# Kernel optimization log

Hardware: AMD Instinct MI355X
Metric: run time of the kernel (lower is better)

## Reference

```python
import jax, jax.numpy as jnp
import numpy as np

DIM = 2048   # token width; == heads*head_dim
H, DH = 16, 128
B, S = 1, 2048
E, K = 4, 2          # routed experts, top-k
HID = 5632           # per-expert SwiGLU hidden: round256(int(2*(4*DIM)/3))
HS = 2816            # shared expert hidden: round256(int(2*(2*DIM)/3))


def setup_inputs() -> dict:
    key = jax.random.key(0)
    ks = jax.random.split(key, 24)
    def g(i, shape, s=0.02):
        return jax.random.normal(ks[i], shape, dtype=jnp.float32) * s
    return {
        "image_tokens": jax.random.normal(ks[0], (B, S, DIM), dtype=jnp.float32),
        "adaln_input": jax.random.normal(ks[1], (B, DIM), dtype=jnp.float32),
        "W_ada": g(2, (DIM, 6 * DIM)), "b_ada": g(3, (6 * DIM,)),
        "Wq": g(4, (DIM, DIM)), "bq": g(5, (DIM,)),
        "Wk": g(6, (DIM, DIM)), "bk": g(7, (DIM,)),
        "Wv": g(8, (DIM, DIM)), "bv": g(9, (DIM,)),
        "q_rms_w": jnp.ones((DIM,), jnp.float32) + g(10, (DIM,)),
        "k_rms_w": jnp.ones((DIM,), jnp.float32) + g(11, (DIM,)),
        "Wo": g(12, (DIM, DIM)), "bo": g(13, (DIM,)),
        "gate_w": g(14, (E, DIM)),
        "We1": g(15, (E, DIM, HID)), "We3": g(16, (E, DIM, HID)), "We2": g(17, (E, HID, DIM)),
        "Ws1": g(18, (DIM, HS)), "Ws3": g(19, (DIM, HS)), "Ws2": g(20, (HS, DIM)),
    }


def _ln(x):  # LayerNorm, elementwise_affine=False, eps=1e-6
    m = jnp.mean(x, -1, keepdims=True)
    v = jnp.var(x, -1, keepdims=True)
    return (x - m) * jax.lax.rsqrt(v + 1e-6)


def _rms(x, w):  # RMSNorm with affine weight, eps=1e-5
    return x * jax.lax.rsqrt(jnp.mean(x * x, -1, keepdims=True) + 1e-5) * w


def reference(image_tokens, adaln_input, W_ada, b_ada, Wq, bq, Wk, bk, Wv, bv,
              q_rms_w, k_rms_w, Wo, bo, gate_w, We1, We3, We2, Ws1, Ws3, Ws2):
    # adaLN: SiLU -> Linear -> 6 chunks, each broadcast as [B,1,dim]
    mod = (jax.nn.silu(adaln_input) @ W_ada + b_ada)[:, None, :]
    sh_msa, sc_msa, g_msa, sh_mlp, sc_mlp, g_mlp = jnp.split(mod, 6, axis=-1)

    # attention branch
    x = _ln(image_tokens) * (1.0 + sc_msa) + sh_msa
    q = _rms(x @ Wq + bq, q_rms_w).reshape(B, S, H, DH)
    k = _rms(x @ Wk + bk, k_rms_w).reshape(B, S, H, DH)
    v = (x @ Wv + bv).reshape(B, S, H, DH)
    att = jax.nn.softmax(jnp.einsum('bihd,bjhd->bhij', q, k) / jnp.sqrt(jnp.float32(DH)), axis=-1)
    o = jnp.einsum('bhij,bjhd->bihd', att, v).reshape(B, S, DIM) @ Wo + bo
    img = g_msa * o + image_tokens

    # MoE SwiGLU FFN branch
    y = _ln(img) * (1.0 + sc_mlp) + sh_mlp
    xf = y.reshape(-1, DIM)                                   # [N, dim]
    scores = jax.nn.softmax(xf @ gate_w.T, axis=-1)           # [N, E]
    tw, ti = jax.lax.top_k(scores, K)                         # no top-k renorm (norm_topk_prob=False)
    comb = jnp.zeros((xf.shape[0], E), xf.dtype).at[jnp.arange(xf.shape[0])[:, None], ti].add(tw)
    h = jax.nn.silu(jnp.einsum('nd,edh->neh', xf, We1)) * jnp.einsum('nd,edh->neh', xf, We3)
    routed = jnp.einsum('neh,ehd,ne->nd', h, We2, comb)
    shared = (jax.nn.silu(xf @ Ws1) * (xf @ Ws3)) @ Ws2
    ff = (routed + shared).reshape(B, S, DIM)

    return g_mlp * ff + img
```

## Files before the change

### kernel.cpp

```cpp
#include <hip/hip_runtime.h>
#include <hip/hip_bf16.h>

typedef unsigned short u16;
typedef __bf16 bf16x8 __attribute__((ext_vector_type(8)));
typedef float f32x4 __attribute__((ext_vector_type(4)));
typedef unsigned short u16x8 __attribute__((ext_vector_type(8)));

constexpr int DIMC = 2048;
constexpr int SEQ = 2048;
constexpr int NHEAD = 16;
constexpr int HDIM = 128;
constexpr int NEXP = 4;
constexpr int HIDC = 5632;
constexpr int HSH = 2816;
constexpr int MOD6 = 6 * DIMC;
constexpr int RSTRIDE = 2304;

static __device__ __forceinline__ u16 f2bf(float f) {
  __hip_bfloat16 b = __float2bfloat16(f);
  return __builtin_bit_cast(u16, b);
}
static __device__ __forceinline__ float bf2f(u16 u) {
  unsigned int x = ((unsigned int)u) << 16;
  return __builtin_bit_cast(float, x);
}
static __device__ __forceinline__ float sigf(float x) { return 1.f / (1.f + __expf(-x)); }
static __device__ __forceinline__ void splitf(float f, u16& h, u16& l) {
  h = f2bf(f);
  l = f2bf(f - bf2f(h));
}

static __device__ __forceinline__ void gload16(const void* src, void* dst) {
  __builtin_amdgcn_global_load_lds((const __attribute__((address_space(1))) void*)src,
                                   (__attribute__((address_space(3))) void*)dst, 16, 0, 0);
}

static __device__ __forceinline__ void xcd_swz(int& bx, int& by, int& bz) {
  const int nx = gridDim.x, ny = gridDim.y;
  const int flat = blockIdx.x + nx * (blockIdx.y + ny * blockIdx.z);
  const int nwg = nx * ny * gridDim.z;
  const int swz = (flat & 7) * (nwg >> 3) + (flat >> 3);
  by = swz % ny;
  const int t = swz / ny;
  bx = t % nx;
  bz = t / nx;
}

static __device__ __forceinline__ float blockSum(float v) {
#pragma unroll
  for (int m = 1; m < 64; m <<= 1) v += __shfl_xor(v, m);
  __shared__ float s[4];
  int w = threadIdx.x >> 6;
  if ((threadIdx.x & 63) == 0) s[w] = v;
  __syncthreads();
  float r = s[0] + s[1] + s[2] + s[3];
  __syncthreads();
  return r;
}

__global__ __launch_bounds__(256) void k_transpose(const float* __restrict__ in, u16* __restrict__ out,
                                                   int R, int C, int ldin, size_t inz, size_t outz) {
  __shared__ __align__(16) float tile[32][33];
  const float* inp = in + (size_t)blockIdx.z * inz;
  u16* outp = out + (size_t)blockIdx.z * outz;
  int tx = threadIdx.x & 31, ty = threadIdx.x >> 5;
  int c0 = blockIdx.x * 32, r0 = blockIdx.y * 32;
#pragma unroll
  for (int i = 0; i < 32; i += 8)
    tile[ty + i][tx] = inp[(size_t)(r0 + ty + i) * ldin + c0 + tx];
  __syncthreads();
#pragma unroll
  for (int i = 0; i < 32; i += 8)
    outp[(size_t)(c0 + ty + i) * R + r0 + tx] = f2bf(tile[tx][ty + i]);
}

__global__ __launch_bounds__(256) void k_transpose_s(const float* __restrict__ in, u16* __restrict__ outh,
                                                     u16* __restrict__ outl, int R, int C, int ldin) {
  __shared__ __align__(16) float tile[32][33];
  int tx = threadIdx.x & 31, ty = threadIdx.x >> 5;
  int c0 = blockIdx.x * 32, r0 = blockIdx.y * 32;
#pragma unroll
  for (int i = 0; i < 32; i += 8)
    tile[ty + i][tx] = in[(size_t)(r0 + ty + i) * ldin + c0 + tx];
  __syncthreads();
#pragma unroll
  for (int i = 0; i < 32; i += 8) {
    float v = tile[tx][ty + i];
    u16 h, l;
    splitf(v, h, l);
    size_t idx = (size_t)(c0 + ty + i) * R + r0 + tx;
    outh[idx] = h;
    outl[idx] = l;
  }
}

__global__ __launch_bounds__(256) void k_adaln_p(const float* __restrict__ a, const float* __restrict__ W,
                                                 float* __restrict__ partial) {
  __shared__ float sa[128];
  int tid = threadIdx.x, slice = blockIdx.y;
  if (tid < 128) { float v = a[slice * 128 + tid]; sa[tid] = v * sigf(v); }
  __syncthreads();
  int j = blockIdx.x * 256 + tid;
  float acc = 0.f;
#pragma unroll 4
  for (int d = 0; d < 128; ++d) acc += sa[d] * W[(size_t)(slice * 128 + d) * MOD6 + j];
  partial[(size_t)slice * MOD6 + j] = acc;
}
__global__ __launch_bounds__(256) void k_adaln_r(const float* __restrict__ partial, const float* __restrict__ b,
                                                 float* __restrict__ mod) {
  int j = blockIdx.x * 256 + threadIdx.x;
  float acc = b[j];
#pragma unroll
  for (int s = 0; s < 16; ++s) acc += partial[(size_t)s * MOD6 + j];
  mod[j] = acc;
}

__global__ __launch_bounds__(256) void k_ln_mod_split(const float* __restrict__ X, const float* __restrict__ mod,
                                                      int shOff, int scOff, u16* __restrict__ outh,
                                                      u16* __restrict__ outl) {
  int row = blockIdx.x, tid = threadIdx.x;
  const float4* x4 = (const float4*)(X + (size_t)row * DIMC);
  float4 v0 = x4[tid * 2], v1 = x4[tid * 2 + 1];
  float s = v0.x + v0.y + v0.z + v0.w + v1.x + v1.y + v1.z + v1.w;
  float ss = v0.x * v0.x + v0.y * v0.y + v0.z * v0.z + v0.w * v0.w +
             v1.x * v1.x + v1.y * v1.y + v1.z * v1.z + v1.w * v1.w;
  s = blockSum(s);
  ss = blockSum(ss);
  float mean = s * (1.f / DIMC);
  float var = ss * (1.f / DIMC) - mean * mean;
  float rstd = rsqrtf(var + 1e-6f);
  const float* sh = mod + shOff;
  const float* sc = mod + scOff;
  int c = tid * 8;
  float xv[8] = {v0.x, v0.y, v0.z, v0.w, v1.x, v1.y, v1.z, v1.w};
  u16x8 oh, ol;
#pragma unroll
  for (int e = 0; e < 8; ++e) {
    float v = (xv[e] - mean) * rstd * (1.f + sc[c + e]) + sh[c + e];
    u16 h, l;
    splitf(v, h, l);
    oh[e] = h;
    ol[e] = l;
  }
  *(u16x8*)(outh + (size_t)row * DIMC + c) = oh;
  *(u16x8*)(outl + (size_t)row * DIMC + c) = ol;
}

__global__ __launch_bounds__(256) void k_ln_mod(const float* __restrict__ X, const float* __restrict__ mod,
                                                int shOff, int scOff, u16* __restrict__ out) {
  int row = blockIdx.x, tid = threadIdx.x;
  const float4* x4 = (const float4*)(X + (size_t)row * DIMC);
  float4 v0 = x4[tid * 2], v1 = x4[tid * 2 + 1];
  float s = v0.x + v0.y + v0.z + v0.w + v1.x + v1.y + v1.z + v1.w;
  float ss = v0.x * v0.x + v0.y * v0.y + v0.z * v0.z + v0.w * v0.w +
             v1.x * v1.x + v1.y * v1.y + v1.z * v1.z + v1.w * v1.w;
  s = blockSum(s);
  ss = blockSum(ss);
  float mean = s * (1.f / DIMC);
  float var = ss * (1.f / DIMC) - mean * mean;
  float rstd = rsqrtf(var + 1e-6f);
  const float* sh = mod + shOff;
  const float* sc = mod + scOff;
  int c = tid * 8;
  float xv[8] = {v0.x, v0.y, v0.z, v0.w, v1.x, v1.y, v1.z, v1.w};
  u16x8 o;
#pragma unroll
  for (int e = 0; e < 8; ++e) o[e] = f2bf((xv[e] - mean) * rstd * (1.f + sc[c + e]) + sh[c + e]);
  *(u16x8*)(out + (size_t)row * DIMC + c) = o;
}

__global__ __launch_bounds__(256) void k_rms_split(const float* __restrict__ X, int ldin,
                                                   const float* __restrict__ w, float scale,
                                                   u16* __restrict__ outh, u16* __restrict__ outl) {
  int row = blockIdx.x, tid = threadIdx.x;
  const float4* x4 = (const float4*)(X + (size_t)row * ldin);
  float4 v0 = x4[tid * 2], v1 = x4[tid * 2 + 1];
  float ss = v0.x * v0.x + v0.y * v0.y + v0.z * v0.z + v0.w * v0.w +
             v1.x * v1.x + v1.y * v1.y + v1.z * v1.z + v1.w * v1.w;
  ss = blockSum(ss);
  float rstd = rsqrtf(ss * (1.f / DIMC) + 1e-5f) * scale;
  int c = tid * 8;
  float xv[8] = {v0.x, v0.y, v0.z, v0.w, v1.x, v1.y, v1.z, v1.w};
  u16x8 oh, ol;
#pragma unroll
  for (int e = 0; e < 8; ++e) {
    float v = xv[e] * rstd * w[c + e];
    u16 h, l;
    splitf(v, h, l);
    oh[e] = h;
    ol[e] = l;
  }
  *(u16x8*)(outh + (size_t)row * DIMC + c) = oh;
  *(u16x8*)(outl + (size_t)row * DIMC + c) = ol;
}

__global__ __launch_bounds__(256) void k_gate(const float* __restrict__ img, const float* __restrict__ mod,
                                              const float* __restrict__ gw, float* __restrict__ comb) {
  int n = blockIdx.x, tid = threadIdx.x;
  const float4* x4 = (const float4*)(img + (size_t)n * DIMC);
  float4 v0 = x4[tid * 2], v1 = x4[tid * 2 + 1];
  float s = v0.x + v0.y + v0.z + v0.w + v1.x + v1.y + v1.z + v1.w;
  float ss = v0.x * v0.x + v0.y * v0.y + v0.z * v0.z + v0.w * v0.w +
             v1.x * v1.x + v1.y * v1.y + v1.z * v1.z + v1.w * v1.w;
  s = blockSum(s);
  ss = blockSum(ss);
  float mean = s * (1.f / DIMC);
  float var = ss * (1.f / DIMC) - mean * mean;
  float rstd = rsqrtf(var + 1e-6f);
  const float* sh = mod + 3 * DIMC;
  const float* sc = mod + 4 * DIMC;
  int c = tid * 8;
  float xv[8] = {v0.x, v0.y, v0.z, v0.w, v1.x, v1.y, v1.z, v1.w};
  float y[8];
#pragma unroll
  for (int e = 0; e < 8; ++e) y[e] = (xv[e] - mean) * rstd * (1.f + sc[c + e]) + sh[c + e];
  float accs[NEXP];
#pragma unroll
  for (int ex = 0; ex < NEXP; ++ex) {
    float a = 0.f;
#pragma unroll
    for (int e = 0; e < 8; ++e) a += y[e] * gw[(size_t)ex * DIMC + c + e];
    accs[ex] = blockSum(a);
  }
  if (tid == 0) {
    float mx = fmaxf(fmaxf(accs[0], accs[1]), fmaxf(accs[2], accs[3]));
    float ex0 = __expf(accs[0] - mx), ex1 = __expf(accs[1] - mx);
    float ex2 = __expf(accs[2] - mx), ex3 = __expf(accs[3] - mx);
    float inv = 1.f / (ex0 + ex1 + ex2 + ex3);
    float v[4] = {ex0 * inv, ex1 * inv, ex2 * inv, ex3 * inv};
    int i1 = 0;
    for (int e = 1; e < 4; ++e)
      if (v[e] > v[i1]) i1 = e;
    int i2 = -1;
    for (int e = 0; e < 4; ++e) {
      if (e == i1) continue;
      if (i2 < 0 || v[e] > v[i2]) i2 = e;
    }
    for (int e = 0; e < 4; ++e) comb[(size_t)n * 4 + e] = (e == i1 || e == i2) ? v[e] : 0.f;
  }
}

__global__ __launch_bounds__(256) void k_route(const float* __restrict__ comb, int* __restrict__ gidx,
                                               float* __restrict__ cw, int* __restrict__ Mpad) {
  int wid = threadIdx.x >> 6, lane = threadIdx.x & 63;
  int base = 0;
  for (int c = 0; c < SEQ; c += 64) {
    int n = c + lane;
    float w = comb[(size_t)n * NEXP + wid];
    bool sel = w > 0.f;
    unsigned long long mask = __ballot(sel);
    int pos = __popcll(mask & ((1ull << lane) - 1ull));
    if (sel) {
      gidx[wid * RSTRIDE + base + pos] = n;
      cw[wid * RSTRIDE + base + pos] = w;
    }
    base += __popcll(mask);
  }
  int padded = (base + 127) & ~127;
  for (int i = base + lane; i < padded; i += 64) {
    gidx[wid * RSTRIDE + i] = -1;
    cw[wid * RSTRIDE + i] = 0.f;
  }
  if (lane == 0) Mpad[wid] = padded;
}

__global__ __launch_bounds__(256, 2) void k_gemmD(const u16* __restrict__ A, const u16* __restrict__ BT,
                                                  int M, int N, int K, float* __restrict__ Cf) {
  int bx, by, bzz;
  xcd_swz(bx, by, bzz);
  __shared__ __align__(16) u16 As[2][8192], Bs[2][8192];
  const int tid = threadIdx.x, wid = tid >> 6, lane = tid & 63;
  const int l16 = lane & 15, g = lane >> 4;
  const int wr = wid >> 1, wc = wid & 1;
  const int m0 = by * 128, n0 = bx * 128;
  const int srow = lane >> 2, scol = (lane & 3) * 8;
  const u16* aS0 = A + (size_t)(m0 + wid * 32 + srow) * K + scol;
  const u16* aS1 = aS0 + (size_t)16 * K;
  const u16* bS0 = BT + (size_t)(n0 + wid * 32 + srow) * K + scol;
  const u16* bS1 = bS0 + (size_t)16 * K;

  const f32x4 zero4 = {0.f, 0.f, 0.f, 0.f};
  f32x4 acc[4][4];
#pragma unroll
  for (int mi = 0; mi < 4; ++mi)
#pragma unroll
    for (int ni = 0; ni < 4; ++ni) acc[mi][ni] = zero4;

  auto stage = [&](int b, int k0) {
    gload16(aS0 + k0, &As[b][wid * 1024]);
    gload16(aS1 + k0, &As[b][wid * 1024 + 512]);
    gload16(aS0 + k0 + 32, &As[b][4096 + wid * 1024]);
    gload16(aS1 + k0 + 32, &As[b][4096 + wid * 1024 + 512]);
    gload16(bS0 + k0, &Bs[b][wid * 1024]);
    gload16(bS1 + k0, &Bs[b][wid * 1024 + 512]);
    gload16(bS0 + k0 + 32, &Bs[b][4096 + wid * 1024]);
    gload16(bS1 + k0 + 32, &Bs[b][4096 + wid * 1024 + 512]);
  };
  auto compute = [&](int b) {
#pragma unroll
    for (int hh = 0; hh < 2; ++hh) {
      const u16* Asrc = &As[b][hh * 4096];
      const u16* Bsrc = &Bs[b][hh * 4096];
      bf16x8 af[4], bfr[4];
#pragma unroll
      for (int mi = 0; mi < 4; ++mi)
        af[mi] = *(const bf16x8*)(&Asrc[(wr * 64 + mi * 16 + l16) * 32 + g * 8]);
#pragma unroll
      for (int ni = 0; ni < 4; ++ni)
        bfr[ni] = *(const bf16x8*)(&Bsrc[(wc * 64 + ni * 16 + l16) * 32 + g * 8]);
#pragma unroll
      for (int mi = 0; mi < 4; ++mi)
#pragma unroll
        for (int ni = 0; ni < 4; ++ni)
          acc[mi][ni] = __builtin_amdgcn_mfma_f32_16x16x32_bf16(af[mi], bfr[ni], acc[mi][ni], 0, 0, 0);
    }
  };

  stage(0, 0);
  __syncthreads();
  for (int k0 = 0; k0 < K; k0 += 128) {
    if (k0 + 64 < K) stage(1, k0 + 64);
    compute(0);
    __syncthreads();
    if (k0 + 128 < K) stage(0, k0 + 128);
    compute(1);
    __syncthreads();
  }

#pragma unroll
  for (int mi = 0; mi < 4; ++mi)
#pragma unroll
    for (int ni = 0; ni < 4; ++ni) {
      const int col = n0 + wc * 64 + ni * 16 + l16;
#pragma unroll
      for (int r = 0; r < 4; ++r) {
        const int row = m0 + wr * 64 + mi * 16 + g * 4 + r;
        Cf[(size_t)row * N + col] = acc[mi][ni][r];
      }
    }
}

template <int GATH>
__global__ __launch_bounds__(256, 2) void k_gemmUP(const u16* __restrict__ A, const u16* __restrict__ B1T0,
                                                   const u16* __restrict__ B3T0, size_t bzs, int N, int K,
                                                   const int* __restrict__ gidx0,
                                                   const float* __restrict__ cw0,
                                                   const int* __restrict__ Mp0, u16* __restrict__ G0,
                                                   size_t cz) {
  int bx, by, bz;
  xcd_swz(bx, by, bz);
  const int z = bz;
  const int m0 = by * 128;
  const int* gidxE = nullptr;
  const float* cwE = nullptr;
  if constexpr (GATH) {
    if (m0 >= Mp0[z]) return;
    gidxE = gidx0 + (size_t)z * RSTRIDE;
    cwE = cw0 + (size_t)z * RSTRIDE;
  }
  const u16* B1T = B1T0 + (size_t)z * bzs;
  const u16* B3T = B3T0 + (size_t)z * bzs;
  u16* G = G0 + (size_t)z * cz;

  __shared__ __align__(16) u16 As[8192], B1s[8192], B3s[8192];
  const int tid = threadIdx.x, wid = tid >> 6, lane = tid & 63;
  const int l16 = lane & 15, g = lane >> 4;
  const int wr = wid >> 1, wc = wid & 1;
  const int n0 = bx * 128;
  const int srow = lane >> 2, scol = (lane & 3) * 8;
  const int slot0 = m0 + wid * 32 + srow;
  int row0, row1;
  if constexpr (GATH) {
    int t0 = gidxE[slot0], t1 = gidxE[slot0 + 16];
    row0 = t0 < 0 ? 0 : t0;
    row1 = t1 < 0 ? 0 : t1;
  } else {
    row0 = slot0;
    row1 = slot0 + 16;
  }
  const u16* aS0 = A + (size_t)row0 * K + scol;
  const u16* aS1 = A + (size_t)row1 * K + scol;
  const u16* b1S0 = B1T + (size_t)(n0 + wid * 32 + srow) * K + scol;
  const u16* b1S1 = b1S0 + (size_t)16 * K;
  const u16* b3S0 = B3T + (size_t)(n0 + wid * 32 + srow) * K + scol;
  const u16* b3S1 = b3S0 + (size_t)16 * K;

  const f32x4 zero4 = {0.f, 0.f, 0.f, 0.f};
  f32x4 acc1[4][4], acc3[4][4];
#pragma unroll
  for (int mi = 0; mi < 4; ++mi)
#pragma unroll
    for (int ni = 0; ni < 4; ++ni) {
      acc1[mi][ni] = zero4;
      acc3[mi][ni] = zero4;
    }

  for (int k0 = 0; k0 < K; k0 += 64) {
    __syncthreads();
    gload16(aS0 + k0, &As[wid * 1024]);
    gload16(aS1 + k0, &As[wid * 1024 + 512]);
    gload16(aS0 + k0 + 32, &As[4096 + wid * 1024]);
    gload16(aS1 + k0 + 32, &As[4096 + wid * 1024 + 512]);
    gload16(b1S0 + k0, &B1s[wid * 1024]);
    gload16(b1S1 + k0, &B1s[wid * 1024 + 512]);
    gload16(b1S0 + k0 + 32, &B1s[4096 + wid * 1024]);
    gload16(b1S1 + k0 + 32, &B1s[4096 + wid * 1024 + 512]);
    gload16(b3S0 + k0, &B3s[wid * 1024]);
    gload16(b3S1 + k0, &B3s[wid * 1024 + 512]);
    gload16(b3S0 + k0 + 32, &B3s[4096 + wid * 1024]);
    gload16(b3S1 + k0 + 32, &B3s[4096 + wid * 1024 + 512]);
    __syncthreads();
#pragma unroll
    for (int hh = 0; hh < 2; ++hh) {
      const u16* Asrc = &As[hh * 4096];
      const u16* B1src = &B1s[hh * 4096];
      const u16* B3src = &B3s[hh * 4096];
      bf16x8 af[4], b1f[4], b3f[4];
#pragma unroll
      for (int mi = 0; mi < 4; ++mi)
        af[mi] = *(const bf16x8*)(&Asrc[(wr * 64 + mi * 16 + l16) * 32 + g * 8]);
#pragma unroll
      for (int ni = 0; ni < 4; ++ni) {
        b1f[ni] = *(const bf16x8*)(&B1src[(wc * 64 + ni * 16 + l16) * 32 + g * 8]);
        b3f[ni] = *(const bf16x8*)(&B3src[(wc * 64 + ni * 16 + l16) * 32 + g * 8]);
      }
#pragma unroll
      for (int mi = 0; mi < 4; ++mi)
#pragma unroll
        for (int ni = 0; ni < 4; ++ni) {
          acc1[mi][ni] = __builtin_amdgcn_mfma_f32_16x16x32_bf16(af[mi], b1f[ni], acc1[mi][ni], 0, 0, 0);
          acc3[mi][ni] = __builtin_amdgcn_mfma_f32_16x16x32_bf16(af[mi], b3f[ni], acc3[mi][ni], 0, 0, 0);
        }
    }
  }

#pragma unroll
  for (int mi = 0; mi < 4; ++mi)
#pragma unroll
    for (int ni = 0; ni < 4; ++ni) {
      const int col = n0 + wc * 64 + ni * 16 + l16;
#pragma unroll
      for (int r = 0; r < 4; ++r) {
        const int slot = m0 + wr * 64 + mi * 16 + g * 4 + r;
        float hv = bf2f(f2bf(acc1[mi][ni][r]));
        float sw = hv * sigf(hv);
        float val = sw * acc3[mi][ni][r];
        if constexpr (GATH) val = val * cwE[slot];
        G[(size_t)slot * N + col] = f2bf(val);
      }
    }
}

__global__ __launch_bounds__(256, 2) void k_gemmR2(const u16* __restrict__ A0, size_t az,
                                                   const u16* __restrict__ BT0, size_t bzs, int N, int K,
                                                   const int* __restrict__ gidx0,
                                                   const int* __restrict__ Mp0, float* __restrict__ ffA,
                                                   float* __restrict__ ffB) {
  int bx, by, bz;
  xcd_swz(bx, by, bz);
  const int z = bz;
  const int m0 = by * 128;
  if (m0 >= Mp0[z]) return;
  const int* gidxE = gidx0 + (size_t)z * RSTRIDE;
  const u16* A = A0 + (size_t)z * az;
  const u16* BT = BT0 + (size_t)z * bzs;
  float* ff = z ? ffB : ffA;

  __shared__ __align__(16) u16 As[2][8192], Bs[2][8192];
  const int tid = threadIdx.x, wid = tid >> 6, lane = tid & 63;
  const int l16 = lane & 15, g = lane >> 4;
  const int wr = wid >> 1, wc = wid & 1;
  const int n0 = bx * 128;
  const int srow = lane >> 2, scol = (lane & 3) * 8;
  const int slot0 = m0 + wid * 32 + srow;
  const u16* aS0 = A + (size_t)slot0 * K + scol;
  const u16* aS1 = A + (size_t)(slot0 + 16) * K + scol;
  const u16* bS0 = BT + (size_t)(n0 + wid * 32 + srow) * K + scol;
  const u16* bS1 = bS0 + (size_t)16 * K;

  const f32x4 zero4 = {0.f, 0.f, 0.f, 0.f};
  f32x4 acc[4][4];
#pragma unroll
  for (int mi = 0; mi < 4; ++mi)
#pragma unroll
    for (int ni = 0; ni < 4; ++ni) acc[mi][ni] = zero4;

  auto stage = [&](int b, int k0) {
    gload16(aS0 + k0, &As[b][wid * 1024]);
    gload16(aS1 + k0, &As[b][wid * 1024 + 512]);
    gload16(aS0 + k0 + 32, &As[b][4096 + wid * 1024]);
    gload16(aS1 + k0 + 32, &As[b][4096 + wid * 1024 + 512]);
    gload16(bS0 + k0, &Bs[b][wid * 1024]);
    gload16(bS1 + k0, &Bs[b][wid * 1024 + 512]);
    gload16(bS0 + k0 + 32, &Bs[b][4096 + wid * 1024]);
    gload16(bS1 + k0 + 32, &Bs[b][4096 + wid * 1024 + 512]);
  };
  auto compute = [&](int b) {
#pragma unroll
    for (int hh = 0; hh < 2; ++hh) {
      const u16* Asrc = &As[b][hh * 4096];
      const u16* Bsrc = &Bs[b][hh * 4096];
      bf16x8 af[4], bfr[4];
#pragma unroll
      for (int mi = 0; mi < 4; ++mi)
        af[mi] = *(const bf16x8*)(&Asrc[(wr * 64 + mi * 16 + l16) * 32 + g * 8]);
#pragma unroll
      for (int ni = 0; ni < 4; ++ni)
        bfr[ni] = *(const bf16x8*)(&Bsrc[(wc * 64 + ni * 16 + l16) * 32 + g * 8]);
#pragma unroll
      for (int mi = 0; mi < 4; ++mi)
#pragma unroll
        for (int ni = 0; ni < 4; ++ni)
          acc[mi][ni] = __builtin_amdgcn_mfma_f32_16x16x32_bf16(af[mi], bfr[ni], acc[mi][ni], 0, 0, 0);
    }
  };

  stage(0, 0);
  __syncthreads();
  for (int k0 = 0; k0 < K; k0 += 128) {
    if (k0 + 64 < K) stage(1, k0 + 64);
    compute(0);
    __syncthreads();
    if (k0 + 128 < K) stage(0, k0 + 128);
    compute(1);
    __syncthreads();
  }

#pragma unroll
  for (int mi = 0; mi < 4; ++mi)
#pragma unroll
    for (int ni = 0; ni < 4; ++ni) {
      const int col = n0 + wc * 64 + ni * 16 + l16;
#pragma unroll
      for (int r = 0; r < 4; ++r) {
        const int slot = m0 + wr * 64 + mi * 16 + g * 4 + r;
        int t = gidxE[slot];
        if (t >= 0) ff[(size_t)t * N + col] += acc[mi][ni][r];
      }
    }
}

template <int MODE>
__global__ __launch_bounds__(256, 2) void k_gemm3s(const u16* __restrict__ Ahg, const u16* __restrict__ Alg,
                                                   const u16* __restrict__ Bhg, const u16* __restrict__ Blg,
                                                   int M, int N, int K, float* __restrict__ Cf,
                                                   const float* __restrict__ bias0,
                                                   const float* __restrict__ bias1,
                                                   const float* __restrict__ bias2,
                                                   const float* __restrict__ gvec,
                                                   const float* __restrict__ resid) {
  int bxs, bys, bzs2;
  xcd_swz(bxs, bys, bzs2);
  __shared__ __align__(16) u16 Ahs[2][4096], Als[2][4096], Bhs[2][4096], Bls[2][4096];
  const int tid = threadIdx.x, wid = tid >> 6, lane = tid & 63;
  const int l16 = lane & 15, g = lane >> 4;
  const int wr = wid >> 1, wc = wid & 1;
  const int m0 = bys * 128, n0 = bxs * 128;
  const int srow = lane >> 2, scol = (lane & 3) * 8;
  const size_t aOff0 = (size_t)(m0 + wid * 32 + srow) * K + scol;
  const size_t aOff1 = aOff0 + (size_t)16 * K;
  const size_t bOff0 = (size_t)(n0 + wid * 32 + srow) * K + scol;
  const size_t bOff1 = bOff0 + (size_t)16 * K;

  const f32x4 zero4 = {0.f, 0.f, 0.f, 0.f};
  f32x4 acc[4][4];
#pragma unroll
  for (int mi = 0; mi < 4; ++mi)
#pragma unroll
    for (int ni = 0; ni < 4; ++ni) acc[mi][ni] = zero4;

  auto stage = [&](int b, int k0) {
    gload16(Ahg + aOff0 + k0, &Ahs[b][wid * 1024]);
    gload16(Ahg + aOff1 + k0, &Ahs[b][wid * 1024 + 512]);
    gload16(Alg + aOff0 + k0, &Als[b][wid * 1024]);
    gload16(Alg + aOff1 + k0, &Als[b][wid * 1024 + 512]);
    gload16(Bhg + bOff0 + k0, &Bhs[b][wid * 1024]);
    gload16(Bhg + bOff1 + k0, &Bhs[b][wid * 1024 + 512]);
    gload16(Blg + bOff0 + k0, &Bls[b][wid * 1024]);
    gload16(Blg + bOff1 + k0, &Bls[b][wid * 1024 + 512]);
  };
  auto compute = [&](int b) {
    bf16x8 bhf[4], blf[4];
#pragma unroll
    for (int ni = 0; ni < 4; ++ni) {
      bhf[ni] = *(const bf16x8*)(&Bhs[b][(wc * 64 + ni * 16 + l16) * 32 + g * 8]);
      blf[ni] = *(const bf16x8*)(&Bls[b][(wc * 64 + ni * 16 + l16) * 32 + g * 8]);
    }
#pragma unroll
    for (int mi = 0; mi < 4; ++mi) {
      bf16x8 ahf = *(const bf16x8*)(&Ahs[b][(wr * 64 + mi * 16 + l16) * 32 + g * 8]);
      bf16x8 alf = *(const bf16x8*)(&Als[b][(wr * 64 + mi * 16 + l16) * 32 + g * 8]);
#pragma unroll
      for (int ni = 0; ni < 4; ++ni) {
        acc[mi][ni] = __builtin_amdgcn_mfma_f32_16x16x32_bf16(alf, bhf[ni], acc[mi][ni], 0, 0, 0);
        acc[mi][ni] = __builtin_amdgcn_mfma_f32_16x16x32_bf16(ahf, blf[ni], acc[mi][ni], 0, 0, 0);
        acc[mi][ni] = __builtin_amdgcn_mfma_f32_16x16x32_bf16(ahf, bhf[ni], acc[mi][ni], 0, 0, 0);
      }
    }
  };

  stage(0, 0);
  __syncthreads();
  for (int k0 = 0; k0 < K; k0 += 64) {
    if (k0 + 32 < K) stage(1, k0 + 32);
    compute(0);
    __syncthreads();
    if (k0 + 64 < K) stage(0, k0 + 64);
    compute(1);
    __syncthreads();
  }

  const float* bp = bias0;
  if constexpr (MODE == 7) bp = (n0 < DIMC) ? bias0 : (n0 < 2 * DIMC ? bias1 : bias2);
#pragma unroll
  for (int mi = 0; mi < 4; ++mi)
#pragma unroll
    for (int ni = 0; ni < 4; ++ni) {
      const int col = n0 + wc * 64 + ni * 16 + l16;
      float bv = bp ? bp[col & (DIMC - 1)] : 0.f;
#pragma unroll
      for (int r = 0; r < 4; ++r) {
        const int row = m0 + wr * 64 + mi * 16 + g * 4 + r;
        float v = acc[mi][ni][r] + bv;
        if constexpr (MODE == 7) {
          Cf[(size_t)row * N + col] = v;
        } else {
          Cf[(size_t)row * N + col] = v * gvec[col] + resid[(size_t)row * N + col];
        }
      }
    }
}

__global__ __launch_bounds__(256, 3) void k_flash3(const u16* __restrict__ qh_g, const u16* __restrict__ ql_g,
                                                   const u16* __restrict__ kh_g, const u16* __restrict__ kl_g,
                                                   const u16* __restrict__ vth_g, const u16* __restrict__ vtl_g,
                                                   u16* __restrict__ oh_g, u16* __restrict__ ol_g) {
  __shared__ __align__(16) u16 Kh[4096], Kl[4096], Vh[128 * 40], Vl[128 * 40];
  __shared__ __align__(16) u16 Pah[4][16 * 40], Pal[4][16 * 40];
  const int tid = threadIdx.x, wid = tid >> 6, lane = tid & 63;
  const int l16 = lane & 15, g = lane >> 4;
  const int bid = blockIdx.x;
  const int h = (bid & 7) + ((bid >> 8) << 3);
  const int qb = (bid >> 3) & 31;
  const int r0 = qb * 64 + wid * 16;
  const size_t hOff = (size_t)h * HDIM;

  bf16x8 qfh[4], qfl[4];
#pragma unroll
  for (int kc = 0; kc < 4; ++kc) {
    const size_t qo = (size_t)(r0 + l16) * DIMC + hOff + kc * 32 + g * 8;
    qfh[kc] = *(const bf16x8*)(qh_g + qo);
    qfl[kc] = *(const bf16x8*)(ql_g + qo);
  }

  const int kr = tid >> 3, ke0 = (tid & 7) * 16;
  const int kswz = (kr & 7) << 4;
  const int kc0 = (ke0 * 2) ^ kswz, kc1 = (ke0 * 2 + 16) ^ kswz;
  char* khp = (char*)Kh + kr * 256;
  char* klp = (char*)Kl + kr * 256;
  const size_t kOff = (size_t)kr * DIMC + hOff + ke0;
  const int vr = tid >> 1, ve0 = (tid & 1) * 16;
  char* vhp = (char*)Vh + vr * 80 + ve0 * 2;
  char* vlp = (char*)Vl + vr * 80 + ve0 * 2;
  const size_t vOff = (size_t)(hOff + vr) * SEQ + ve0;

  u16x8 kH0, kH1, kL0, kL1, vH0, vH1, vL0, vL1;
  kH0 = *(const u16x8*)(kh_g + kOff);
  kH1 = *(const u16x8*)(kh_g + kOff + 8);
  kL0 = *(const u16x8*)(kl_g + kOff);
  kL1 = *(const u16x8*)(kl_g + kOff + 8);
  vH0 = *(const u16x8*)(vth_g + vOff);
  vH1 = *(const u16x8*)(vth_g + vOff + 8);
  vL0 = *(const u16x8*)(vtl_g + vOff);
  vL1 = *(const u16x8*)(vtl_g + vOff + 8);

  const f32x4 zero4 = {0.f, 0.f, 0.f, 0.f};
  f32x4 oacc[8];
#pragma unroll
  for (int db = 0; db < 8; ++db) oacc[db] = zero4;
  float mr[4], lr[4];
#pragma unroll
  for (int r = 0; r < 4; ++r) {
    mr[r] = -3.0e38f;
    lr[r] = 0.f;
  }

  for (int j0 = 0; j0 < SEQ; j0 += 32) {
    __syncthreads();
    *(u16x8*)(khp + kc0) = kH0;
    *(u16x8*)(khp + kc1) = kH1;
    *(u16x8*)(klp + kc0) = kL0;
    *(u16x8*)(klp + kc1) = kL1;
    *(u16x8*)(vhp) = vH0;
    *(u16x8*)(vhp + 16) = vH1;
    *(u16x8*)(vlp) = vL0;
    *(u16x8*)(vlp + 16) = vL1;
    __syncthreads();
    if (j0 + 32 < SEQ) {
      const size_t ko = kOff + (size_t)(j0 + 32) * DIMC;
      const size_t vo = vOff + j0 + 32;
      kH0 = *(const u16x8*)(kh_g + ko);
      kH1 = *(const u16x8*)(kh_g + ko + 8);
      kL0 = *(const u16x8*)(kl_g + ko);
      kL1 = *(const u16x8*)(kl_g + ko + 8);
      vH0 = *(const u16x8*)(vth_g + vo);
      vH1 = *(const u16x8*)(vth_g + vo + 8);
      vL0 = *(const u16x8*)(vtl_g + vo);
      vL1 = *(const u16x8*)(vtl_g + vo + 8);
    }
    f32x4 s0 = zero4, s1 = zero4;
    __builtin_amdgcn_s_setprio(1);
#pragma unroll
    for (int kc = 0; kc < 4; ++kc) {
      const int cb = (kc * 64 + g * 16) ^ ((l16 & 7) << 4);
      bf16x8 kh0 = *(const bf16x8*)((char*)Kh + l16 * 256 + cb);
      bf16x8 kl0 = *(const bf16x8*)((char*)Kl + l16 * 256 + cb);
      bf16x8 kh1 = *(const bf16x8*)((char*)Kh + (16 + l16) * 256 + cb);
      bf16x8 kl1 = *(const bf16x8*)((char*)Kl + (16 + l16) * 256 + cb);
      s0 = __builtin_amdgcn_mfma_f32_16x16x32_bf16(qfl[kc], kh0, s0, 0, 0, 0);
      s0 = __builtin_amdgcn_mfma_f32_16x16x32_bf16(qfh[kc], kl0, s0, 0, 0, 0);
      s0 = __builtin_amdgcn_mfma_f32_16x16x32_bf16(qfh[kc], kh0, s0, 0, 0, 0);
      s1 = __builtin_amdgcn_mfma_f32_16x16x32_bf16(qfl[kc], kh1, s1, 0, 0, 0);
      s1 = __builtin_amdgcn_mfma_f32_16x16x32_bf16(qfh[kc], kl1, s1, 0, 0, 0);
      s1 = __builtin_amdgcn_mfma_f32_16x16x32_bf16(qfh[kc], kh1, s1, 0, 0, 0);
    }
    __builtin_amdgcn_s_setprio(0);
    float corr[4];
#pragma unroll
    for (int r = 0; r < 4; ++r) {
      float tm = fmaxf(s0[r], s1[r]);
#pragma unroll
      for (int m = 1; m < 16; m <<= 1) tm = fmaxf(tm, __shfl_xor(tm, m));
      float mn = fmaxf(mr[r], tm);
      corr[r] = __expf(mr[r] - mn);
      mr[r] = mn;
      float p0 = __expf(s0[r] - mn);
      float p1 = __expf(s1[r] - mn);
      lr[r] = lr[r] * corr[r] + p0 + p1;
      u16 p0h = f2bf(p0), p1h = f2bf(p1);
      Pah[wid][(g * 4 + r) * 40 + l16] = p0h;
      Pah[wid][(g * 4 + r) * 40 + 16 + l16] = p1h;
      Pal[wid][(g * 4 + r) * 40 + l16] = f2bf(p0 - bf2f(p0h));
      Pal[wid][(g * 4 + r) * 40 + 16 + l16] = f2bf(p1 - bf2f(p1h));
    }
#pragma unroll
    for (int db = 0; db < 8; ++db)
#pragma unroll
      for (int r = 0; r < 4; ++r) oacc[db][r] *= corr[r];
    bf16x8 pfh = *(const bf16x8*)(&Pah[wid][l16 * 40 + g * 8]);
    bf16x8 pfl = *(const bf16x8*)(&Pal[wid][l16 * 40 + g * 8]);
    __builtin_amdgcn_s_setprio(1);
#pragma unroll
    for (int db = 0; db < 8; ++db) {
      const int row = db * 16 + l16;
      bf16x8 vh = *(const bf16x8*)((char*)Vh + row * 80 + g * 16);
      bf16x8 vl = *(const bf16x8*)((char*)Vl + row * 80 + g * 16);
      oacc[db] = __builtin_amdgcn_mfma_f32_16x16x32_bf16(pfl, vh, oacc[db], 0, 0, 0);
      oacc[db] = __builtin_amdgcn_mfma_f32_16x16x32_bf16(pfh, vl, oacc[db], 0, 0, 0);
      oacc[db] = __builtin_amdgcn_mfma_f32_16x16x32_bf16(pfh, vh, oacc[db], 0, 0, 0);
    }
    __builtin_amdgcn_s_setprio(0);
  }
#pragma unroll
  for (int r = 0; r < 4; ++r) {
#pragma unroll
    for (int m = 1; m < 16; m <<= 1) lr[r] += __shfl_xor(lr[r], m);
    lr[r] = 1.f / lr[r];
  }
#pragma unroll
  for (int db = 0; db < 8; ++db)
#pragma unroll
    for (int r = 0; r < 4; ++r) {
      float v = oacc[db][r] * lr[r];
      u16 hh, ll;
      splitf(v, hh, ll);
      const size_t idx = (size_t)(r0 + g * 4 + r) * DIMC + hOff + db * 16 + l16;
      oh_g[idx] = hh;
      ol_g[idx] = ll;
    }
}

__global__ __launch_bounds__(256) void k_final(const float* __restrict__ ffA, const float* __restrict__ ffB,
                                               const float* img, const float* __restrict__ mod,
                                               float* out) {
  const float4* gm = (const float4*)(mod + 5 * DIMC);
  const int total = SEQ * DIMC / 4;
  const int stride = gridDim.x * blockDim.x;
  for (int i = blockIdx.x * blockDim.x + threadIdx.x; i < total; i += stride) {
    int col4 = i & (DIMC / 4 - 1);
    float4 gv = gm[col4];
    float4 fa = ((const float4*)ffA)[i];
    float4 fb = ((const float4*)ffB)[i];
    float4 iv = ((const float4*)img)[i];
    float4 ov;
    ov.x = gv.x * (fa.x + fb.x) + iv.x;
    ov.y = gv.y * (fa.y + fb.y) + iv.y;
    ov.z = gv.z * (fa.z + fb.z) + iv.z;
    ov.w = gv.w * (fa.w + fb.w) + iv.w;
    ((float4*)out)[i] = ov;
  }
}

extern "C" void kernel_launch(void* const* d_in, const int* in_sizes, int n_in, void* d_out, int out_size,
                              void* d_ws, size_t ws_size, hipStream_t stream) {
  (void)in_sizes; (void)n_in; (void)out_size; (void)ws_size;
  const float* image_tokens = (const float*)d_in[0];
  const float* adaln_input = (const float*)d_in[1];
  const float* W_ada = (const float*)d_in[2];
  const float* b_ada = (const float*)d_in[3];
  const float* Wq = (const float*)d_in[4];
  const float* bq = (const float*)d_in[5];
  const float* Wk = (const float*)d_in[6];
  const float* bk = (const float*)d_in[7];
  const float* Wv = (const float*)d_in[8];
  const float* bv = (const float*)d_in[9];
  const float* q_rms_w = (const float*)d_in[10];
  const float* k_rms_w = (const float*)d_in[11];
  const float* Wo = (const float*)d_in[12];
  const float* bo = (const float*)d_in[13];
  const float* gate_w = (const float*)d_in[14];
  const float* We1 = (const float*)d_in[15];
  const float* We3 = (const float*)d_in[16];
  const float* We2 = (const float*)d_in[17];
  const float* Ws1 = (const float*)d_in[18];
  const float* Ws3 = (const float*)d_in[19];
  const float* Ws2 = (const float*)d_in[20];

  char* cur = (char*)d_ws;
  auto alloc = [&](size_t n) {
    char* p = cur;
    cur += (n + 255) & ~(size_t)255;
    return p;
  };
  float* modv = (float*)alloc((size_t)MOD6 * 4);
  float* adap = (float*)alloc((size_t)16 * MOD6 * 4);
  float* comb = (float*)alloc((size_t)SEQ * NEXP * 4);
  int* gidx = (int*)alloc((size_t)NEXP * RSTRIDE * 4);
  float* cw = (float*)alloc((size_t)NEXP * RSTRIDE * 4);
  int* Mpad = (int*)alloc((size_t)NEXP * 4);
  u16* xh = (u16*)alloc((size_t)SEQ * DIMC * 2);
  u16* xl = (u16*)alloc((size_t)SEQ * DIMC * 2);
  u16* wTh3 = (u16*)alloc((size_t)3 * DIMC * DIMC * 2);
  u16* wTl3 = (u16*)alloc((size_t)3 * DIMC * DIMC * 2);
  float* tf3 = (float*)alloc((size_t)SEQ * 3 * DIMC * 4);
  u16* qhb = (u16*)alloc((size_t)SEQ * DIMC * 2);
  u16* qlb = (u16*)alloc((size_t)SEQ * DIMC * 2);
  u16* khb = (u16*)alloc((size_t)SEQ * DIMC * 2);
  u16* klb = (u16*)alloc((size_t)SEQ * DIMC * 2);
  u16* vth = (u16*)alloc((size_t)SEQ * DIMC * 2);
  u16* vtl = (u16*)alloc((size_t)SEQ * DIMC * 2);
  u16* aoh = (u16*)alloc((size_t)SEQ * DIMC * 2);
  u16* aol = (u16*)alloc((size_t)SEQ * DIMC * 2);
  u16* x_act = (u16*)alloc((size_t)SEQ * DIMC * 2);
  float* ff = (float*)alloc((size_t)SEQ * DIMC * 4);
  float* ffB = (float*)alloc((size_t)SEQ * DIMC * 4);
  float* img = (float*)d_out;
  const size_t BZ = (size_t)HIDC * DIMC;
  const size_t CZ = (size_t)RSTRIDE * HIDC;
  u16* moe0 = xh;
  u16* wbufE1 = moe0;
  u16* wbufE3 = moe0 + 2 * BZ;
  u16* G2 = moe0 + 4 * BZ;
  u16* wbufS1 = moe0;
  u16* wbufS3 = moe0 + (size_t)HSH * DIMC;
  u16* wbufS2 = moe0 + (size_t)2 * HSH * DIMC;
  u16* Gs = moe0 + (size_t)3 * HSH * DIMC;

  dim3 blk(256);

  k_adaln_p<<<dim3(MOD6 / 256, 16), blk, 0, stream>>>(adaln_input, W_ada, adap);
  k_adaln_r<<<dim3(MOD6 / 256), blk, 0, stream>>>(adap, b_ada, modv);

  k_ln_mod_split<<<dim3(SEQ), blk, 0, stream>>>(image_tokens, modv, 0, DIMC, xh, xl);
  k_transpose_s<<<dim3(DIMC / 32, DIMC / 32), blk, 0, stream>>>(Wq, wTh3, wTl3, DIMC, DIMC, DIMC);
  k_transpose_s<<<dim3(DIMC / 32, DIMC / 32), blk, 0, stream>>>(
      Wk, wTh3 + (size_t)DIMC * DIMC, wTl3 + (size_t)DIMC * DIMC, DIMC, DIMC, DIMC);
  k_transpose_s<<<dim3(DIMC / 32, DIMC / 32), blk, 0, stream>>>(
      Wv, wTh3 + (size_t)2 * DIMC * DIMC, wTl3 + (size_t)2 * DIMC * DIMC, DIMC, DIMC, DIMC);
  k_gemm3s<7><<<dim3(3 * DIMC / 128, SEQ / 128), blk, 0, stream>>>(
      xh, xl, wTh3, wTl3, SEQ, 3 * DIMC, DIMC, tf3, bq, bk, bv, nullptr, nullptr);
  k_rms_split<<<dim3(SEQ), blk, 0, stream>>>(tf3, 3 * DIMC, q_rms_w, 0.08838834764831845f, qhb, qlb);
  k_rms_split<<<dim3(SEQ), blk, 0, stream>>>(tf3 + DIMC, 3 * DIMC, k_rms_w, 1.f, khb, klb);
  k_transpose_s<<<dim3(DIMC / 32, SEQ / 32), blk, 0, stream>>>(tf3 + 2 * DIMC, vth, vtl, SEQ, DIMC,
                                                               3 * DIMC);
  k_flash3<<<dim3(SEQ / 64 * NHEAD), blk, 0, stream>>>(qhb, qlb, khb, klb, vth, vtl, aoh, aol);
  k_transpose_s<<<dim3(DIMC / 32, DIMC / 32), blk, 0, stream>>>(Wo, wTh3, wTl3, DIMC, DIMC, DIMC);
  k_gemm3s<2><<<dim3(DIMC / 128, SEQ / 128), blk, 0, stream>>>(
      aoh, aol, wTh3, wTl3, SEQ, DIMC, DIMC, img, bo, nullptr, nullptr, modv + 2 * DIMC, image_tokens);

  k_ln_mod<<<dim3(SEQ), blk, 0, stream>>>(img, modv, 3 * DIMC, 4 * DIMC, x_act);
  k_gate<<<dim3(SEQ), blk, 0, stream>>>(img, modv, gate_w, comb);
  k_route<<<dim3(1), blk, 0, stream>>>(comb, gidx, cw, Mpad);
  hipMemsetAsync(ffB, 0, (size_t)SEQ * DIMC * 4, stream);

  k_transpose<<<dim3(HSH / 32, DIMC / 32), blk, 0, stream>>>(Ws1, wbufS1, DIMC, HSH, HSH, 0, 0);
  k_transpose<<<dim3(HSH / 32, DIMC / 32), blk, 0, stream>>>(Ws3, wbufS3, DIMC, HSH, HSH, 0, 0);
  k_gemmUP<0><<<dim3(HSH / 128, SEQ / 128, 1), blk, 0, stream>>>(
      x_act, wbufS1, wbufS3, 0, HSH, DIMC, nullptr, nullptr, nullptr, Gs, 0);
  k_transpose<<<dim3(DIMC / 32, HSH / 32), blk, 0, stream>>>(Ws2, wbufS2, HSH, DIMC, DIMC, 0, 0);
  k_gemmD<<<dim3(DIMC / 128, SEQ / 128), blk, 0, stream>>>(Gs, wbufS2, SEQ, DIMC, HSH, ff);

  const size_t WE = (size_t)DIMC * HIDC;
  for (int p = 0; p < 2; ++p) {
    const int e0 = p * 2;
    k_transpose<<<dim3(HIDC / 32, DIMC / 32, 2), blk, 0, stream>>>(We1 + (size_t)e0 * WE, wbufE1,
                                                                   DIMC, HIDC, HIDC, WE, BZ);
    k_transpose<<<dim3(HIDC / 32, DIMC / 32, 2), blk, 0, stream>>>(We3 + (size_t)e0 * WE, wbufE3,
                                                                   DIMC, HIDC, HIDC, WE, BZ);
    k_gemmUP<1><<<dim3(HIDC / 128, SEQ / 128, 2), blk, 0, stream>>>(
        x_act, wbufE1, wbufE3, BZ, HIDC, DIMC, gidx + e0 * RSTRIDE, cw + e0 * RSTRIDE, Mpad + e0, G2,
        CZ);
    k_transpose<<<dim3(DIMC / 32, HIDC / 32, 2), blk, 0, stream>>>(We2 + (size_t)e0 * WE, wbufE1,
                                                                   HIDC, DIMC, DIMC, WE, BZ);
    k_gemmR2<<<dim3(DIMC / 128, SEQ / 128, 2), blk, 0, stream>>>(
        G2, CZ, wbufE1, BZ, DIMC, HIDC, gidx + e0 * RSTRIDE, Mpad + e0, ff, ffB);
  }

  k_final<<<dim3(1024), blk, 0, stream>>>(ff, ffB, img, modv, (float*)d_out);
}
```

Before: 1.372 ms.

## Double-buffer the fused up-projection GEMM so loads overlap MFMA compute

Restructures the k_gemmUP main loop from load-sync-compute of a 64-wide K chunk into a ping-pong of two 32-wide shared buffers. Loads for the next half-tile are issued before computing the current one, which hides global-load latency behind the MFMAs. Launch bounds are raised from 2 to 3 blocks per SM to improve occupancy. The catch is more barriers per K step and tighter register pressure, since 32 accumulators must fit the 3-block budget, which could cause spills.

```diff
diff --git a/kernel.cpp b/kernel.cpp
--- a/kernel.cpp
+++ b/kernel.cpp
@@ -341,7 +341,7 @@
 }
 
 template <int GATH>
-__global__ __launch_bounds__(256, 2) void k_gemmUP(const u16* __restrict__ A, const u16* __restrict__ B1T0,
+__global__ __launch_bounds__(256, 3) void k_gemmUP(const u16* __restrict__ A, const u16* __restrict__ B1T0,
                                                    const u16* __restrict__ B3T0, size_t bzs, int N, int K,
                                                    const int* __restrict__ gidx0,
                                                    const float* __restrict__ cw0,
@@ -362,7 +362,7 @@
   const u16* B3T = B3T0 + (size_t)z * bzs;
   u16* G = G0 + (size_t)z * cz;
 
-  __shared__ __align__(16) u16 As[8192], B1s[8192], B3s[8192];
+  __shared__ __align__(16) u16 As[2][4096], B1s[2][4096], B3s[2][4096];
   const int tid = threadIdx.x, wid = tid >> 6, lane = tid & 63;
   const int l16 = lane & 15, g = lane >> 4;
   const int wr = wid >> 1, wc = wid & 1;
@@ -395,43 +395,42 @@
       acc3[mi][ni] = zero4;
     }
 
+  auto stage = [&](int b, int k0) {
+    gload16(aS0 + k0, &As[b][wid * 1024]);
+    gload16(aS1 + k0, &As[b][wid * 1024 + 512]);
+    gload16(b1S0 + k0, &B1s[b][wid * 1024]);
+    gload16(b1S1 + k0, &B1s[b][wid * 1024 + 512]);
+    gload16(b3S0 + k0, &B3s[b][wid * 1024]);
+    gload16(b3S1 + k0, &B3s[b][wid * 1024 + 512]);
+  };
+  auto compute = [&](int b) {
+    bf16x8 af[4], b1f[4], b3f[4];
+#pragma unroll
+    for (int mi = 0; mi < 4; ++mi)
+      af[mi] = *(const bf16x8*)(&As[b][(wr * 64 + mi * 16 + l16) * 32 + g * 8]);
+#pragma unroll
+    for (int ni = 0; ni < 4; ++ni) {
+      b1f[ni] = *(const bf16x8*)(&B1s[b][(wc * 64 + ni * 16 + l16) * 32 + g * 8]);
+      b3f[ni] = *(const bf16x8*)(&B3s[b][(wc * 64 + ni * 16 + l16) * 32 + g * 8]);
+    }
+#pragma unroll
+    for (int mi = 0; mi < 4; ++mi)
+#pragma unroll
+      for (int ni = 0; ni < 4; ++ni) {
+        acc1[mi][ni] = __builtin_amdgcn_mfma_f32_16x16x32_bf16(af[mi], b1f[ni], acc1[mi][ni], 0, 0, 0);
+        acc3[mi][ni] = __builtin_amdgcn_mfma_f32_16x16x32_bf16(af[mi], b3f[ni], acc3[mi][ni], 0, 0, 0);
+      }
+  };
+
+  stage(0, 0);
+  __syncthreads();
   for (int k0 = 0; k0 < K; k0 += 64) {
+    if (k0 + 32 < K) stage(1, k0 + 32);
+    compute(0);
     __syncthreads();
-    gload16(aS0 + k0, &As[wid * 1024]);
-    gload16(aS1 + k0, &As[wid * 1024 + 512]);
-    gload16(aS0 + k0 + 32, &As[4096 + wid * 1024]);
-    gload16(aS1 + k0 + 32, &As[4096 + wid * 1024 + 512]);
-    gload16(b1S0 + k0, &B1s[wid * 1024]);
-    gload16(b1S1 + k0, &B1s[wid * 1024 + 512]);
-    gload16(b1S0 + k0 + 32, &B1s[4096 + wid * 1024]);
-    gload16(b1S1 + k0 + 32, &B1s[4096 + wid * 1024 + 512]);
-    gload16(b3S0 + k0, &B3s[wid * 1024]);
-    gload16(b3S1 + k0, &B3s[wid * 1024 + 512]);
-    gload16(b3S0 + k0 + 32, &B3s[4096 + wid * 1024]);
-    gload16(b3S1 + k0 + 32, &B3s[4096 + wid * 1024 + 512]);
+    if (k0 + 64 < K) stage(0, k0 + 64);
+    compute(1);
     __syncthreads();
-#pragma unroll
-    for (int hh = 0; hh < 2; ++hh) {
-      const u16* Asrc = &As[hh * 4096];
-      const u16* B1src = &B1s[hh * 4096];
-      const u16* B3src = &B3s[hh * 4096];
-      bf16x8 af[4], b1f[4], b3f[4];
-#pragma unroll
-      for (int mi = 0; mi < 4; ++mi)
-        af[mi] = *(const bf16x8*)(&Asrc[(wr * 64 + mi * 16 + l16) * 32 + g * 8]);
-#pragma unroll
-      for (int ni = 0; ni < 4; ++ni) {
-        b1f[ni] = *(const bf16x8*)(&B1src[(wc * 64 + ni * 16 + l16) * 32 + g * 8]);
-        b3f[ni] = *(const bf16x8*)(&B3src[(wc * 64 + ni * 16 + l16) * 32 + g * 8]);
-      }
-#pragma unroll
-      for (int mi = 0; mi < 4; ++mi)
-#pragma unroll
-        for (int ni = 0; ni < 4; ++ni) {
-          acc1[mi][ni] = __builtin_amdgcn_mfma_f32_16x16x32_bf16(af[mi], b1f[ni], acc1[mi][ni], 0, 0, 0);
-          acc3[mi][ni] = __builtin_amdgcn_mfma_f32_16x16x32_bf16(af[mi], b3f[ni], acc3[mi][ni], 0, 0, 0);
-        }
-    }
   }
 
 #pragma unroll
```

Result: slower. 1.934 ms (+40.9%).
